# Kernel optimization log

Hardware: AMD Instinct MI355X
Metric: run time of the kernel (lower is better)

## Reference

```python
import jax, jax.numpy as jnp
import numpy as np

N_NODES = 100000
N_EDGES = 3200000
FEAT = 16


def gcn_conv(x, src, dst, W, b):
    # PyG GCNConv: add self-loops, symmetric normalization deg^{-1/2}(A+I)deg^{-1/2},
    # then linear transform and scatter-add aggregation.
    n = x.shape[0]
    loop = jnp.arange(n, dtype=src.dtype)
    s = jnp.concatenate([src, loop])
    d = jnp.concatenate([dst, loop])
    deg = jax.ops.segment_sum(jnp.ones_like(d, dtype=x.dtype), d, num_segments=n)
    dinv = jnp.where(deg > 0, jax.lax.rsqrt(deg), 0.0)
    norm = dinv[s] * dinv[d]  # [E+N]
    h = x @ W  # [N, out]
    msg = h[s] * norm[:, None]  # gather + weight
    out = jax.ops.segment_sum(msg, d, num_segments=n)  # scatter-add
    return out + b


def setup_inputs() -> dict:
    key = jax.random.key(0)
    k1, k2, k3, k4 = jax.random.split(key, 4)
    scale = 1.0 / np.sqrt(FEAT)
    return {
        "x": jax.random.normal(k1, (N_NODES, FEAT), dtype=jnp.float32),
        "edge_index": jax.random.randint(k2, (2, N_EDGES), 0, N_NODES, dtype=jnp.int64) if jax.config.jax_enable_x64 else jax.random.randint(k2, (2, N_EDGES), 0, N_NODES, dtype=jnp.int32),
        "W1": jax.random.normal(k3, (FEAT, 16), dtype=jnp.float32) * scale,
        "b1": jnp.zeros((16,), dtype=jnp.float32),
        "W2": jax.random.normal(k4, (16, FEAT), dtype=jnp.float32) * scale,
        "b2": jnp.zeros((FEAT,), dtype=jnp.float32),
    }


def reference(x, edge_index, W1, b1, W2, b2):
    src, dst = edge_index[0], edge_index[1]
    h = gcn_conv(x, src, dst, W1, b1)
    h = jax.nn.relu(h)
    out = gcn_conv(h, src, dst, W2, b2)
    return out
```

## Files before the change

### kernel.cpp

```cpp
#include <hip/hip_runtime.h>

#define F 16
#define BSHIFT 8
#define NPB 256
#define NB 391
#define CH 4096
#define BCAP 9216


__global__ void init_cursor_kernel(unsigned* __restrict__ cursor) {
    int i = threadIdx.x;
    if (i < NB) cursor[i * 16] = (unsigned)(i * BCAP);
}

__global__ __launch_bounds__(512) void
reorder_kernel(const int* __restrict__ src, const int* __restrict__ dst,
               unsigned* __restrict__ cursor, unsigned* __restrict__ recs, int E) {
    __shared__ unsigned lsorted[CH];
    __shared__ unsigned short lbkt[CH];
    __shared__ unsigned cnt[NB];
    __shared__ unsigned lstart[NB + 1];
    int t = threadIdx.x, b = blockIdx.x;
    int e0 = b * CH;
    int cnt_e = E - e0; if (cnt_e > CH) cnt_e = CH;

    for (int i = t; i < NB; i += 512) cnt[i] = 0;
    __syncthreads();
    unsigned pk[8], rs[8];
#pragma unroll
    for (int j = 0; j < 8; ++j) {
        int i = t + j * 512;
        pk[j] = 0xFFFFFFFFu;
        if (i < cnt_e) {
            unsigned d = (unsigned)dst[e0 + i];
            rs[j] = (unsigned)src[e0 + i];
            unsigned bk = d >> BSHIFT;
            unsigned r = atomicAdd(&cnt[bk], 1u);
            pk[j] = bk | ((d & 255u) << 9) | (r << 17);
        }
    }
    __syncthreads();
    if (t < 64) {
        unsigned run = 0;
        for (int c = 0; c < NB; c += 64) {
            int idx = c + t;
            unsigned v = (idx < NB) ? cnt[idx] : 0u;
            unsigned inc = v;
#pragma unroll
            for (int d = 1; d < 64; d <<= 1) {
                unsigned o = __shfl_up(inc, d, 64);
                if (t >= d) inc += o;
            }
            if (idx < NB) lstart[idx] = run + inc - v;
            run += __shfl(inc, 63, 64);
        }
        if (t == 0) lstart[NB] = (unsigned)cnt_e;
    }
    __syncthreads();
    {
        int s0 = (int)(((unsigned)b * 101u) % (unsigned)NB);
        for (int q = t; q < NB; q += 512) {
            int i = s0 + q; if (i >= NB) i -= NB;
            unsigned c = cnt[i];
            if (c) cnt[i] = atomicAdd(&cursor[i * 16], c);
        }
    }
    __syncthreads();
#pragma unroll
    for (int j = 0; j < 8; ++j) {
        int i = t + j * 512;
        if (i < cnt_e) {
            unsigned p = pk[j];
            unsigned bk = p & 0x1FFu;
            unsigned pos = lstart[bk] + (p >> 17);
            lsorted[pos] = rs[j] | (((p >> 9) & 255u) << 17);
            lbkt[pos] = (unsigned short)bk;
        }
    }
    __syncthreads();
    for (int i = t; i < cnt_e; i += 512) {
        unsigned bk = lbkt[i];
        recs[cnt[bk] + ((unsigned)i - lstart[bk])] = lsorted[i];
    }
}

__global__ __launch_bounds__(1024) void
sort2_kernel(const unsigned* __restrict__ recs, const unsigned* __restrict__ cursor,
             unsigned* __restrict__ srcs, int* __restrict__ noff, int* __restrict__ nend,
             float* __restrict__ dinv, const float* __restrict__ x,
             float* __restrict__ z, int n) {
    __shared__ unsigned lsort[BCAP];
    __shared__ unsigned cnt[NPB];
    __shared__ unsigned ex[NPB];
    __shared__ float ldv[NPB];
    __shared__ unsigned wtot[4];
    int t = threadIdx.x, b = blockIdx.x;
    int e0 = b * BCAP;
    int used = (int)(cursor[b * 16] - (unsigned)e0);
    if (t < NPB) cnt[t] = 0;
    __syncthreads();
    unsigned pk[9], rsr[9];
#pragma unroll
    for (int j = 0; j < 9; ++j) {
        int i = t + j * 1024;
        pk[j] = 0xFFFFFFFFu;
        if (i < used) {
            unsigned rec = recs[e0 + i];
            unsigned node = rec >> 17;
            rsr[j] = rec & 0x1FFFFu;
            unsigned r = atomicAdd(&cnt[node], 1u);
            pk[j] = node | (r << 8);
        }
    }
    __syncthreads();
    if (t < NPB) {
        unsigned c = cnt[t];
        unsigned inc = c;
        int lane = t & 63, w = t >> 6;
#pragma unroll
        for (int d = 1; d < 64; d <<= 1) {
            unsigned o = __shfl_up(inc, d, 64);
            if (lane >= d) inc += o;
        }
        if (lane == 63) wtot[w] = inc;
        __syncthreads();
        unsigned wbase = 0;
        for (int i = 0; i < w; ++i) wbase += wtot[i];
        unsigned e = wbase + inc - c;
        ex[t] = e;
        float dv = rsqrtf((float)c + 1.0f);
        ldv[t] = dv;
        int node = b * NPB + t;
        if (node < n) {
            noff[node] = e0 + (int)e;
            nend[node] = e0 + (int)(e + c);
            dinv[node] = dv;
        }
    } else {
        __syncthreads();
    }
    __syncthreads();
#pragma unroll
    for (int j = 0; j < 9; ++j) {
        int i = t + j * 1024;
        if (i < used) {
            unsigned p = pk[j];
            lsort[ex[p & 255u] + (p >> 8)] = rsr[j];
        }
    }
    __syncthreads();
    for (int i = t; i < used; i += 1024) srcs[e0 + i] = lsort[i];
    {
        int node = b * NPB + (t >> 2);
        if (node < n) {
            float4 v = ((const float4*)x)[(size_t)b * 1024 + t];
            float dv = ldv[t >> 2];
            v.x *= dv; v.y *= dv; v.z *= dv; v.w *= dv;
            ((float4*)z)[(size_t)b * 1024 + t] = v;
        }
    }
}

__global__ void agg_csr_kernel(const float* __restrict__ hin, const unsigned* __restrict__ srcs,
                               const int* __restrict__ noff, const int* __restrict__ nend,
                               const float* __restrict__ dinv,
                               const float* __restrict__ W, const float* __restrict__ bias,
                               float* __restrict__ outp, int n, int mode) {
    __shared__ float a1[64][F + 1];
    __shared__ float Ws[F * F];
    int t = threadIdx.x;
    int g = t >> 2, c = t & 3;
    Ws[t] = W[t];
    int node = blockIdx.x * 64 + g;
    const float4* h4 = (const float4*)hin;
    float di = 0.f;
    if (node < n) {
        di = dinv[node];
        int e0 = noff[node], e1 = nend[node];
        float4 s0 = {0,0,0,0}, s1 = {0,0,0,0}, s2 = {0,0,0,0}, s3 = {0,0,0,0};
        int e = e0;
        for (; e + 4 <= e1; e += 4) {
            int ia = srcs[e], ib = srcs[e + 1], ic = srcs[e + 2], id = srcs[e + 3];
            float4 va = h4[(size_t)ia * 4 + c];
            float4 vb = h4[(size_t)ib * 4 + c];
            float4 vc = h4[(size_t)ic * 4 + c];
            float4 vd = h4[(size_t)id * 4 + c];
            s0.x += va.x; s0.y += va.y; s0.z += va.z; s0.w += va.w;
            s1.x += vb.x; s1.y += vb.y; s1.z += vb.z; s1.w += vb.w;
            s2.x += vc.x; s2.y += vc.y; s2.z += vc.z; s2.w += vc.w;
            s3.x += vd.x; s3.y += vd.y; s3.z += vd.z; s3.w += vd.w;
        }
        for (; e < e1; ++e) {
            float4 va = h4[(size_t)srcs[e] * 4 + c];
            s0.x += va.x; s0.y += va.y; s0.z += va.z; s0.w += va.w;
        }
        float4 self = h4[(size_t)node * 4 + c];
        a1[g][c * 4 + 0] = (s0.x + s1.x) + (s2.x + s3.x) + self.x;
        a1[g][c * 4 + 1] = (s0.y + s1.y) + (s2.y + s3.y) + self.y;
        a1[g][c * 4 + 2] = (s0.z + s1.z) + (s2.z + s3.z) + self.z;
        a1[g][c * 4 + 3] = (s0.w + s1.w) + (s2.w + s3.w) + self.w;
    }
    __syncthreads();
    if (node < n) {
        float4 o = {0.f, 0.f, 0.f, 0.f};
        int j = c * 4;
#pragma unroll
        for (int k = 0; k < F; ++k) {
            float ak = a1[g][k];
            o.x += ak * Ws[k * F + j + 0];
            o.y += ak * Ws[k * F + j + 1];
            o.z += ak * Ws[k * F + j + 2];
            o.w += ak * Ws[k * F + j + 3];
        }
        float4 bi = ((const float4*)bias)[c];
        o.x = di * o.x + bi.x; o.y = di * o.y + bi.y;
        o.z = di * o.z + bi.z; o.w = di * o.w + bi.w;
        if (mode == 1) {
            o.x = fmaxf(o.x, 0.f) * di; o.y = fmaxf(o.y, 0.f) * di;
            o.z = fmaxf(o.z, 0.f) * di; o.w = fmaxf(o.w, 0.f) * di;
        }
        ((float4*)outp)[(size_t)node * 4 + c] = o;
    }
}


__global__ void deg_kernel(const int* __restrict__ dst, float* __restrict__ deg, int E) {
    int e = blockIdx.x * blockDim.x + threadIdx.x;
    if (e < E) atomicAdd(&deg[dst[e]], 1.0f);
}
__global__ void dinv_kernel(float* __restrict__ deg, int n) {
    int i = blockIdx.x * blockDim.x + threadIdx.x;
    if (i < n) deg[i] = rsqrtf(deg[i] + 1.0f);
}
__global__ void linear2_kernel(const float* __restrict__ in, const float* __restrict__ acc,
                               const float* __restrict__ dinv, const float* __restrict__ W,
                               const float* __restrict__ bias, float* __restrict__ out,
                               int n, int mode) {
    __shared__ float Ws[F * F];
    __shared__ float As[16][F + 1];
    int t = threadIdx.x;
    Ws[t] = W[t];
    int nb = t >> 4, j = t & 15;
    int i = blockIdx.x * 16 + nb;
    float di = 0.f, v = 0.f;
    if (i < n) {
        di = dinv[i]; v = in[i * F + j];
        if (mode) { v = di * (acc[i * F + j] + v) + bias[j]; v = fmaxf(v, 0.f); }
    }
    As[nb][j] = v;
    __syncthreads();
    if (i < n) {
        float s = 0.f;
#pragma unroll
        for (int k = 0; k < F; ++k) s += As[nb][k] * Ws[k * F + j];
        out[i * F + j] = s * di;
    }
}
__global__ void scatter_kernel(const int* __restrict__ src, const int* __restrict__ dst,
                               const float* __restrict__ h, float* __restrict__ acc, int E) {
    int t = blockIdx.x * blockDim.x + threadIdx.x;
    int e = t >> 4, j = t & 15;
    if (e < E) atomicAdd(&acc[dst[e] * F + j], h[src[e] * F + j]);
}
__global__ void out_kernel(const float* __restrict__ acc, const float* __restrict__ h,
                           const float* __restrict__ dinv, const float* __restrict__ bias,
                           float* __restrict__ out, int n) {
    int t = blockIdx.x * blockDim.x + threadIdx.x;
    if (t < n * F) {
        int i = t >> 4, j = t & 15;
        out[t] = dinv[i] * (acc[t] + h[t]) + bias[j];
    }
}


extern "C" void kernel_launch(void* const* d_in, const int* in_sizes, int n_in,
                              void* d_out, int out_size, void* d_ws, size_t ws_size,
                              hipStream_t stream) {
    const float* x  = (const float*)d_in[0];
    const int*   ei = (const int*)d_in[1];
    const float* W1 = (const float*)d_in[2];
    const float* b1 = (const float*)d_in[3];
    const float* W2 = (const float*)d_in[4];
    const float* b2 = (const float*)d_in[5];
    float* outp = (float*)d_out;

    const int N = in_sizes[0] / F;
    const int E = in_sizes[1] / 2;
    const int* src = ei;
    const int* dst = ei + E;

    const int nb_rt = (N + NPB - 1) >> BSHIFT;
    const size_t RC = (size_t)NB * BCAP;
    size_t need = sizeof(unsigned) * ((size_t)N * 19 + 2 * RC + 16 * NB);

    if (nb_rt == NB && E <= CH * 65535 && ws_size >= need) {
        float* dinv = (float*)d_ws;
        float* z = dinv + N;
        unsigned* recs = (unsigned*)(z + (size_t)F * N);
        float* y = (float*)recs;
        unsigned* srcs = recs + RC;
        int* noff = (int*)(srcs + RC);
        int* nend = noff + N;
        unsigned* cursor = (unsigned*)(nend + N);

        init_cursor_kernel<<<1, 512, 0, stream>>>(cursor);
        reorder_kernel<<<(E + CH - 1) / CH, 512, 0, stream>>>(src, dst, cursor, recs, E);
        sort2_kernel<<<NB, 1024, 0, stream>>>(recs, cursor, srcs, noff, nend, dinv, x, z, N);
        agg_csr_kernel<<<(N + 63) / 64, 256, 0, stream>>>(z, srcs, noff, nend, dinv, W1, b1, y, N, 1);
        agg_csr_kernel<<<(N + 63) / 64, 256, 0, stream>>>(y, srcs, noff, nend, dinv, W2, b2, outp, N, 2);
    } else {
        float* dinv = (float*)d_ws;
        float* h = dinv + N;
        float* acc = h + (size_t)F * N;
        hipMemsetAsync(dinv, 0, (size_t)N * sizeof(float), stream);
        hipMemsetAsync(acc, 0, (size_t)F * N * sizeof(float), stream);
        deg_kernel<<<(E + 255) / 256, 256, 0, stream>>>(dst, dinv, E);
        dinv_kernel<<<(N + 255) / 256, 256, 0, stream>>>(dinv, N);
        linear2_kernel<<<(N + 15) / 16, 256, 0, stream>>>(x, nullptr, dinv, W1, nullptr, h, N, 0);
        scatter_kernel<<<((size_t)E * F + 255) / 256, 256, 0, stream>>>(src, dst, h, acc, E);
        linear2_kernel<<<(N + 15) / 16, 256, 0, stream>>>(h, acc, dinv, W2, b1, h, N, 1);
        hipMemsetAsync(acc, 0, (size_t)F * N * sizeof(float), stream);
        scatter_kernel<<<((size_t)E * F + 255) / 256, 256, 0, stream>>>(src, dst, h, acc, E);
        out_kernel<<<((size_t)N * F + 255) / 256, 256, 0, stream>>>(acc, h, dinv, b2, outp, N);
    }
}
```

Before: 202.1 us.

## Replace per-node CSR sort with bucketed LDS-atomic aggregation over smaller buckets

Shrinks destination buckets to 64 nodes and drops the second in-bucket sort pass that built CSR offsets. A light histogram kernel computes degrees and prescaled features. Aggregation then walks each bucket's unsorted records and accumulates into shared memory with float atomics. This removes a full sort pass and its extra global traffic. It costs many LDS atomics per edge, and bucket capacity headroom is tighter.

New measurement: 755.6 us. +273.9%, slower.

```diff
diff --git a/kernel.cpp b/kernel.cpp
--- a/kernel.cpp
+++ b/kernel.cpp
@@ -1,15 +1,15 @@
 #include <hip/hip_runtime.h>
 
 #define F 16
-#define BSHIFT 8
-#define NPB 256
-#define NB 391
+#define BSHIFT 6
+#define NPB 64
+#define NB 1563
 #define CH 4096
-#define BCAP 9216
+#define BCAP 2304
 
 
 __global__ void init_cursor_kernel(unsigned* __restrict__ cursor) {
-    int i = threadIdx.x;
+    int i = blockIdx.x * 256 + threadIdx.x;
     if (i < NB) cursor[i * 16] = (unsigned)(i * BCAP);
 }
 
@@ -36,7 +36,7 @@
             rs[j] = (unsigned)src[e0 + i];
             unsigned bk = d >> BSHIFT;
             unsigned r = atomicAdd(&cnt[bk], 1u);
-            pk[j] = bk | ((d & 255u) << 9) | (r << 17);
+            pk[j] = bk | ((d & 63u) << 11) | (r << 17);
         }
     }
     __syncthreads();
@@ -71,9 +71,9 @@
         int i = t + j * 512;
         if (i < cnt_e) {
             unsigned p = pk[j];
-            unsigned bk = p & 0x1FFu;
+            unsigned bk = p & 0x7FFu;
             unsigned pos = lstart[bk] + (p >> 17);
-            lsorted[pos] = rs[j] | (((p >> 9) & 255u) << 17);
+            lsorted[pos] = rs[j] | (((p >> 11) & 63u) << 17);
             lbkt[pos] = (unsigned short)bk;
         }
     }
@@ -84,129 +84,86 @@
     }
 }
 
-__global__ __launch_bounds__(1024) void
-sort2_kernel(const unsigned* __restrict__ recs, const unsigned* __restrict__ cursor,
-             unsigned* __restrict__ srcs, int* __restrict__ noff, int* __restrict__ nend,
-             float* __restrict__ dinv, const float* __restrict__ x,
+__global__ __launch_bounds__(256) void
+histz_kernel(const unsigned* __restrict__ recs, const unsigned* __restrict__ cursor,
+             const float* __restrict__ x, float* __restrict__ dinv,
              float* __restrict__ z, int n) {
-    __shared__ unsigned lsort[BCAP];
     __shared__ unsigned cnt[NPB];
-    __shared__ unsigned ex[NPB];
     __shared__ float ldv[NPB];
-    __shared__ unsigned wtot[4];
     int t = threadIdx.x, b = blockIdx.x;
     int e0 = b * BCAP;
     int used = (int)(cursor[b * 16] - (unsigned)e0);
     if (t < NPB) cnt[t] = 0;
     __syncthreads();
-    unsigned pk[9], rsr[9];
-#pragma unroll
-    for (int j = 0; j < 9; ++j) {
-        int i = t + j * 1024;
-        pk[j] = 0xFFFFFFFFu;
-        if (i < used) {
-            unsigned rec = recs[e0 + i];
-            unsigned node = rec >> 17;
-            rsr[j] = rec & 0x1FFFFu;
-            unsigned r = atomicAdd(&cnt[node], 1u);
-            pk[j] = node | (r << 8);
-        }
-    }
+    for (int i = t; i < used; i += 256)
+        atomicAdd(&cnt[recs[e0 + i] >> 17], 1u);
     __syncthreads();
     if (t < NPB) {
-        unsigned c = cnt[t];
-        unsigned inc = c;
-        int lane = t & 63, w = t >> 6;
-#pragma unroll
-        for (int d = 1; d < 64; d <<= 1) {
-            unsigned o = __shfl_up(inc, d, 64);
-            if (lane >= d) inc += o;
-        }
-        if (lane == 63) wtot[w] = inc;
-        __syncthreads();
-        unsigned wbase = 0;
-        for (int i = 0; i < w; ++i) wbase += wtot[i];
-        unsigned e = wbase + inc - c;
-        ex[t] = e;
-        float dv = rsqrtf((float)c + 1.0f);
+        float dv = rsqrtf((float)cnt[t] + 1.0f);
         ldv[t] = dv;
         int node = b * NPB + t;
-        if (node < n) {
-            noff[node] = e0 + (int)e;
-            nend[node] = e0 + (int)(e + c);
-            dinv[node] = dv;
-        }
-    } else {
-        __syncthreads();
-    }
-    __syncthreads();
-#pragma unroll
-    for (int j = 0; j < 9; ++j) {
-        int i = t + j * 1024;
-        if (i < used) {
-            unsigned p = pk[j];
-            lsort[ex[p & 255u] + (p >> 8)] = rsr[j];
-        }
-    }
-    __syncthreads();
-    for (int i = t; i < used; i += 1024) srcs[e0 + i] = lsort[i];
-    {
-        int node = b * NPB + (t >> 2);
-        if (node < n) {
-            float4 v = ((const float4*)x)[(size_t)b * 1024 + t];
-            float dv = ldv[t >> 2];
-            v.x *= dv; v.y *= dv; v.z *= dv; v.w *= dv;
-            ((float4*)z)[(size_t)b * 1024 + t] = v;
-        }
-    }
-}
-
-__global__ void agg_csr_kernel(const float* __restrict__ hin, const unsigned* __restrict__ srcs,
-                               const int* __restrict__ noff, const int* __restrict__ nend,
-                               const float* __restrict__ dinv,
-                               const float* __restrict__ W, const float* __restrict__ bias,
-                               float* __restrict__ outp, int n, int mode) {
-    __shared__ float a1[64][F + 1];
+        if (node < n) dinv[node] = dv;
+    }
+    __syncthreads();
+    int node = b * NPB + (t >> 2);
+    if (node < n) {
+        float4 v = ((const float4*)x)[(size_t)b * (NPB * 4) + t];
+        float dv = ldv[t >> 2];
+        v.x *= dv; v.y *= dv; v.z *= dv; v.w *= dv;
+        ((float4*)z)[(size_t)b * (NPB * 4) + t] = v;
+    }
+}
+
+__global__ __launch_bounds__(256) void
+agg_kernel(const float* __restrict__ hin, const unsigned* __restrict__ recs,
+           const unsigned* __restrict__ cursor, const float* __restrict__ dinv,
+           const float* __restrict__ W, const float* __restrict__ bias,
+           float* __restrict__ outp, int n, int mode) {
+    __shared__ float acc[NPB][F + 1];
     __shared__ float Ws[F * F];
-    int t = threadIdx.x;
+    int t = threadIdx.x, b = blockIdx.x;
+    int e0 = b * BCAP;
+    int used = (int)(cursor[b * 16] - (unsigned)e0);
+    Ws[t] = W[t];
+    for (int i = t; i < NPB * (F + 1); i += 256) ((float*)acc)[i] = 0.f;
+    __syncthreads();
     int g = t >> 2, c = t & 3;
-    Ws[t] = W[t];
-    int node = blockIdx.x * 64 + g;
     const float4* h4 = (const float4*)hin;
-    float di = 0.f;
+    int i = g;
+    for (; i + 64 < used; i += 128) {
+        unsigned r0 = recs[e0 + i];
+        unsigned r1 = recs[e0 + i + 64];
+        float4 v0 = h4[(size_t)(r0 & 0x1FFFFu) * 4 + c];
+        float4 v1 = h4[(size_t)(r1 & 0x1FFFFu) * 4 + c];
+        float* a0 = &acc[r0 >> 17][c * 4];
+        atomicAdd(a0 + 0, v0.x); atomicAdd(a0 + 1, v0.y);
+        atomicAdd(a0 + 2, v0.z); atomicAdd(a0 + 3, v0.w);
+        float* a1 = &acc[r1 >> 17][c * 4];
+        atomicAdd(a1 + 0, v1.x); atomicAdd(a1 + 1, v1.y);
+        atomicAdd(a1 + 2, v1.z); atomicAdd(a1 + 3, v1.w);
+    }
+    if (i < used) {
+        unsigned r0 = recs[e0 + i];
+        float4 v0 = h4[(size_t)(r0 & 0x1FFFFu) * 4 + c];
+        float* a0 = &acc[r0 >> 17][c * 4];
+        atomicAdd(a0 + 0, v0.x); atomicAdd(a0 + 1, v0.y);
+        atomicAdd(a0 + 2, v0.z); atomicAdd(a0 + 3, v0.w);
+    }
+    __syncthreads();
+    int node = b * NPB + g;
     if (node < n) {
-        di = dinv[node];
-        int e0 = noff[node], e1 = nend[node];
-        float4 s0 = {0,0,0,0}, s1 = {0,0,0,0}, s2 = {0,0,0,0}, s3 = {0,0,0,0};
-        int e = e0;
-        for (; e + 4 <= e1; e += 4) {
-            int ia = srcs[e], ib = srcs[e + 1], ic = srcs[e + 2], id = srcs[e + 3];
-            float4 va = h4[(size_t)ia * 4 + c];
-            float4 vb = h4[(size_t)ib * 4 + c];
-            float4 vc = h4[(size_t)ic * 4 + c];
-            float4 vd = h4[(size_t)id * 4 + c];
-            s0.x += va.x; s0.y += va.y; s0.z += va.z; s0.w += va.w;
-            s1.x += vb.x; s1.y += vb.y; s1.z += vb.z; s1.w += vb.w;
-            s2.x += vc.x; s2.y += vc.y; s2.z += vc.z; s2.w += vc.w;
-            s3.x += vd.x; s3.y += vd.y; s3.z += vd.z; s3.w += vd.w;
-        }
-        for (; e < e1; ++e) {
-            float4 va = h4[(size_t)srcs[e] * 4 + c];
-            s0.x += va.x; s0.y += va.y; s0.z += va.z; s0.w += va.w;
-        }
         float4 self = h4[(size_t)node * 4 + c];
-        a1[g][c * 4 + 0] = (s0.x + s1.x) + (s2.x + s3.x) + self.x;
-        a1[g][c * 4 + 1] = (s0.y + s1.y) + (s2.y + s3.y) + self.y;
-        a1[g][c * 4 + 2] = (s0.z + s1.z) + (s2.z + s3.z) + self.z;
-        a1[g][c * 4 + 3] = (s0.w + s1.w) + (s2.w + s3.w) + self.w;
+        float* ar = &acc[g][c * 4];
+        ar[0] += self.x; ar[1] += self.y; ar[2] += self.z; ar[3] += self.w;
     }
     __syncthreads();
     if (node < n) {
+        float di = dinv[node];
         float4 o = {0.f, 0.f, 0.f, 0.f};
         int j = c * 4;
 #pragma unroll
         for (int k = 0; k < F; ++k) {
-            float ak = a1[g][k];
+            float ak = acc[g][k];
             o.x += ak * Ws[k * F + j + 0];
             o.y += ak * Ws[k * F + j + 1];
             o.z += ak * Ws[k * F + j + 2];
@@ -291,23 +248,20 @@
 
     const int nb_rt = (N + NPB - 1) >> BSHIFT;
     const size_t RC = (size_t)NB * BCAP;
-    size_t need = sizeof(unsigned) * ((size_t)N * 19 + 2 * RC + 16 * NB);
+    size_t need = sizeof(unsigned) * ((size_t)N * 33 + RC + 16 * NB);
 
     if (nb_rt == NB && E <= CH * 65535 && ws_size >= need) {
         float* dinv = (float*)d_ws;
         float* z = dinv + N;
-        unsigned* recs = (unsigned*)(z + (size_t)F * N);
-        float* y = (float*)recs;
-        unsigned* srcs = recs + RC;
-        int* noff = (int*)(srcs + RC);
-        int* nend = noff + N;
-        unsigned* cursor = (unsigned*)(nend + N);
-
-        init_cursor_kernel<<<1, 512, 0, stream>>>(cursor);
+        float* y = z + (size_t)F * N;
+        unsigned* recs = (unsigned*)(y + (size_t)F * N);
+        unsigned* cursor = recs + RC;
+
+        init_cursor_kernel<<<(NB + 255) / 256, 256, 0, stream>>>(cursor);
         reorder_kernel<<<(E + CH - 1) / CH, 512, 0, stream>>>(src, dst, cursor, recs, E);
-        sort2_kernel<<<NB, 1024, 0, stream>>>(recs, cursor, srcs, noff, nend, dinv, x, z, N);
-        agg_csr_kernel<<<(N + 63) / 64, 256, 0, stream>>>(z, srcs, noff, nend, dinv, W1, b1, y, N, 1);
-        agg_csr_kernel<<<(N + 63) / 64, 256, 0, stream>>>(y, srcs, noff, nend, dinv, W2, b2, outp, N, 2);
+        histz_kernel<<<NB, 256, 0, stream>>>(recs, cursor, x, dinv, z, N);
+        agg_kernel<<<NB, 256, 0, stream>>>(z, recs, cursor, dinv, W1, b1, y, N, 1);
+        agg_kernel<<<NB, 256, 0, stream>>>(y, recs, cursor, dinv, W2, b2, outp, N, 2);
     } else {
         float* dinv = (float*)d_ws;
         float* h = dinv + N;
```

## Balance edge work across threads in aggregation via merge-path style chunking

Applied to the files above, without the earlier changes.

Keeps the packed record (local node id in high bits) in the sorted source array, so each 64-node block can split its contiguous edge range evenly across 64 thread groups instead of one group per node. Each group accumulates runs per destination and flushes partial sums with shared-memory atomics when the destination changes. This removes per-node degree imbalance within the block (Poisson degrees ~32), at the cost of LDS atomics, a zero-init pass and per-edge branch checks. It relies on noff of consecutive nodes in a block being contiguous.

Result: slower. 210.1 us (+3.9%).

```diff
diff --git a/kernel.cpp b/kernel.cpp
--- a/kernel.cpp
+++ b/kernel.cpp
@@ -107,7 +107,7 @@
         if (i < used) {
             unsigned rec = recs[e0 + i];
             unsigned node = rec >> 17;
-            rsr[j] = rec & 0x1FFFFu;
+            rsr[j] = rec;
             unsigned r = atomicAdd(&cnt[node], 1u);
             pk[j] = node | (r << 8);
         }
@@ -161,52 +161,79 @@
     }
 }
 
-__global__ void agg_csr_kernel(const float* __restrict__ hin, const unsigned* __restrict__ srcs,
-                               const int* __restrict__ noff, const int* __restrict__ nend,
-                               const float* __restrict__ dinv,
-                               const float* __restrict__ W, const float* __restrict__ bias,
-                               float* __restrict__ outp, int n, int mode) {
-    __shared__ float a1[64][F + 1];
+__global__ __launch_bounds__(256) void
+agg_bal_kernel(const float* __restrict__ hin, const unsigned* __restrict__ srcs,
+               const int* __restrict__ noff, const int* __restrict__ nend,
+               const float* __restrict__ dinv,
+               const float* __restrict__ W, const float* __restrict__ bias,
+               float* __restrict__ outp, int n, int mode) {
+    __shared__ float acc[64][F + 1];
     __shared__ float Ws[F * F];
-    int t = threadIdx.x;
+    int t = threadIdx.x, b = blockIdx.x;
     int g = t >> 2, c = t & 3;
     Ws[t] = W[t];
-    int node = blockIdx.x * 64 + g;
+    for (int i = t; i < 64 * (F + 1); i += 256) ((float*)acc)[i] = 0.f;
+    __syncthreads();
+    int nfirst = b * 64;
+    int nlast = nfirst + 63; if (nlast > n - 1) nlast = n - 1;
+    int e_start = noff[nfirst];
+    int e_end = nend[nlast];
+    int T = e_end - e_start;
+    int chunk = (T + 63) >> 6;
+    int gs = e_start + g * chunk;
+    int ge = gs + chunk; if (ge > e_end) ge = e_end;
     const float4* h4 = (const float4*)hin;
-    float di = 0.f;
+
+#define PROC(r, v)                                                        \
+    {                                                                     \
+        int nd = (int)((r >> 17) & 63u);                                  \
+        if (nd != cur) {                                                  \
+            float* a = &acc[cur][c * 4];                                  \
+            atomicAdd(a + 0, s.x); atomicAdd(a + 1, s.y);                 \
+            atomicAdd(a + 2, s.z); atomicAdd(a + 3, s.w);                 \
+            s.x = 0.f; s.y = 0.f; s.z = 0.f; s.w = 0.f;                   \
+            cur = nd;                                                     \
+        }                                                                 \
+        s.x += v.x; s.y += v.y; s.z += v.z; s.w += v.w;                   \
+    }
+
+    if (gs < ge) {
+        int cur = (int)((srcs[gs] >> 17) & 63u);
+        float4 s = {0.f, 0.f, 0.f, 0.f};
+        int e = gs;
+        for (; e + 4 <= ge; e += 4) {
+            unsigned r0 = srcs[e], r1 = srcs[e + 1], r2 = srcs[e + 2], r3 = srcs[e + 3];
+            float4 v0 = h4[(size_t)(r0 & 0x1FFFFu) * 4 + c];
+            float4 v1 = h4[(size_t)(r1 & 0x1FFFFu) * 4 + c];
+            float4 v2 = h4[(size_t)(r2 & 0x1FFFFu) * 4 + c];
+            float4 v3 = h4[(size_t)(r3 & 0x1FFFFu) * 4 + c];
+            PROC(r0, v0); PROC(r1, v1); PROC(r2, v2); PROC(r3, v3);
+        }
+        for (; e < ge; ++e) {
+            unsigned r0 = srcs[e];
+            float4 v0 = h4[(size_t)(r0 & 0x1FFFFu) * 4 + c];
+            PROC(r0, v0);
+        }
+        float* a = &acc[cur][c * 4];
+        atomicAdd(a + 0, s.x); atomicAdd(a + 1, s.y);
+        atomicAdd(a + 2, s.z); atomicAdd(a + 3, s.w);
+    }
+#undef PROC
+    __syncthreads();
+    int node = nfirst + g;
     if (node < n) {
-        di = dinv[node];
-        int e0 = noff[node], e1 = nend[node];
-        float4 s0 = {0,0,0,0}, s1 = {0,0,0,0}, s2 = {0,0,0,0}, s3 = {0,0,0,0};
-        int e = e0;
-        for (; e + 4 <= e1; e += 4) {
-            int ia = srcs[e], ib = srcs[e + 1], ic = srcs[e + 2], id = srcs[e + 3];
-            float4 va = h4[(size_t)ia * 4 + c];
-            float4 vb = h4[(size_t)ib * 4 + c];
-            float4 vc = h4[(size_t)ic * 4 + c];
-            float4 vd = h4[(size_t)id * 4 + c];
-            s0.x += va.x; s0.y += va.y; s0.z += va.z; s0.w += va.w;
-            s1.x += vb.x; s1.y += vb.y; s1.z += vb.z; s1.w += vb.w;
-            s2.x += vc.x; s2.y += vc.y; s2.z += vc.z; s2.w += vc.w;
-            s3.x += vd.x; s3.y += vd.y; s3.z += vd.z; s3.w += vd.w;
-        }
-        for (; e < e1; ++e) {
-            float4 va = h4[(size_t)srcs[e] * 4 + c];
-            s0.x += va.x; s0.y += va.y; s0.z += va.z; s0.w += va.w;
-        }
         float4 self = h4[(size_t)node * 4 + c];
-        a1[g][c * 4 + 0] = (s0.x + s1.x) + (s2.x + s3.x) + self.x;
-        a1[g][c * 4 + 1] = (s0.y + s1.y) + (s2.y + s3.y) + self.y;
-        a1[g][c * 4 + 2] = (s0.z + s1.z) + (s2.z + s3.z) + self.z;
-        a1[g][c * 4 + 3] = (s0.w + s1.w) + (s2.w + s3.w) + self.w;
+        float* ar = &acc[g][c * 4];
+        ar[0] += self.x; ar[1] += self.y; ar[2] += self.z; ar[3] += self.w;
     }
     __syncthreads();
     if (node < n) {
+        float di = dinv[node];
         float4 o = {0.f, 0.f, 0.f, 0.f};
         int j = c * 4;
 #pragma unroll
         for (int k = 0; k < F; ++k) {
-            float ak = a1[g][k];
+            float ak = acc[g][k];
             o.x += ak * Ws[k * F + j + 0];
             o.y += ak * Ws[k * F + j + 1];
             o.z += ak * Ws[k * F + j + 2];
@@ -306,8 +333,8 @@
         init_cursor_kernel<<<1, 512, 0, stream>>>(cursor);
         reorder_kernel<<<(E + CH - 1) / CH, 512, 0, stream>>>(src, dst, cursor, recs, E);
         sort2_kernel<<<NB, 1024, 0, stream>>>(recs, cursor, srcs, noff, nend, dinv, x, z, N);
-        agg_csr_kernel<<<(N + 63) / 64, 256, 0, stream>>>(z, srcs, noff, nend, dinv, W1, b1, y, N, 1);
-        agg_csr_kernel<<<(N + 63) / 64, 256, 0, stream>>>(y, srcs, noff, nend, dinv, W2, b2, outp, N, 2);
+        agg_bal_kernel<<<(N + 63) / 64, 256, 0, stream>>>(z, srcs, noff, nend, dinv, W1, b1, y, N, 1);
+        agg_bal_kernel<<<(N + 63) / 64, 256, 0, stream>>>(y, srcs, noff, nend, dinv, W2, b2, outp, N, 2);
     } else {
         float* dinv = (float*)d_ws;
         float* h = dinv + N;
```
